# Performance work log

Measured on AMD Instinct MI355X. Metric: run time of the kernel, lower is better.

Reference implementation:

```python
import jax, jax.numpy as jnp
import numpy as np

N, D, Q, C_IN, C = 8192, 32, 4096, 128, 256
EPS = 1e-5

def _bn(h, g, b):
    # training-mode BatchNorm1d (biased variance, as torch uses for normalization)
    mu = h.mean(0)
    var = ((h - mu) ** 2).mean(0)
    return (h - mu) * jax.lax.rsqrt(var + EPS) * g + b

def setup_inputs():
    key = jax.random.key(0)
    cnt = iter(range(1000))
    def w(shape, s=0.05):
        return jax.random.normal(jax.random.fold_in(key, next(cnt)), shape, jnp.float32) * s
    ones = lambda n: jnp.ones((n,), jnp.float32)
    zeros = lambda n: jnp.zeros((n,), jnp.float32)
    rng = np.random.default_rng(0)
    block = N // D
    # padded neighbor table: rows sorted & duplicate-free (one neighbor per id-block)
    nbr_np = (np.arange(D)[None, :] * block + rng.integers(0, block, size=(N, D))).astype(np.int64)
    src = np.repeat(np.arange(N, dtype=np.int64), D)
    edge_index = jnp.asarray(np.stack([src, nbr_np.reshape(-1)]))
    E = edge_index.shape[1]
    C2 = 2 * C
    return {
        'x': w((N, C_IN), 1.0),
        'edge_index': edge_index,
        'edge_weight': jax.random.uniform(jax.random.fold_in(key, 999), (E,), jnp.float32, 0.5, 1.5),
        'edge_label_index': jnp.asarray(rng.integers(0, N, size=(2, Q)).astype(np.int64)),
        'nbr': jnp.asarray(nbr_np),
        'pe_gamma': ones(C_IN), 'pe_beta': zeros(C_IN),
        'W_pe': w((C_IN, C)), 'b_pe': zeros(C),
        'W_gcn': w((C, C)), 'b_gcn': zeros(C), 'bn1_g': ones(C), 'bn1_b': zeros(C),
        'Wq': w((C, C)), 'bq': zeros(C), 'Wk': w((C, C)), 'bk': zeros(C),
        'Wv': w((C, C)), 'bv': zeros(C), 'Wo': w((C, C)), 'bo': zeros(C),
        'bn2_g': ones(C), 'bn2_b': zeros(C),
        'W_m1': w((C, C2)), 'b_m1': zeros(C2), 'W_m2': w((C2, C)), 'b_m2': zeros(C),
        'bn3_g': ones(C), 'bn3_b': zeros(C),
        'W_cm': w((C, C)), 'b_cm': zeros(C), 'W_sm': w((C, C)), 'b_sm': zeros(C),
        'W_o1': w((C2, C)), 'b_o1': zeros(C), 'bno_g': ones(C), 'bno_b': zeros(C),
        'W_o2': w((C, 1)), 'b_o2': zeros(1),
        't': jnp.ones((), jnp.float32),
    }

def reference(x, edge_index, edge_weight, edge_label_index, nbr,
              pe_gamma, pe_beta, W_pe, b_pe,
              W_gcn, b_gcn, bn1_g, bn1_b,
              Wq, bq, Wk, bk, Wv, bv, Wo, bo, bn2_g, bn2_b,
              W_m1, b_m1, W_m2, b_m2, bn3_g, bn3_b,
              W_cm, b_cm, W_sm, b_sm,
              W_o1, b_o1, bno_g, bno_b, W_o2, b_o2, t):
    src, dst = edge_index[0], edge_index[1]
    h = _bn(x, pe_gamma, pe_beta) @ W_pe + b_pe                       # [N, C]
    # --- GPSConv layer: local GCN (self-loops) + global attention + MLP ---
    deg = jnp.zeros((N,), h.dtype).at[dst].add(edge_weight) + 1.0     # self-loop weight 1
    dinv = jax.lax.rsqrt(deg)
    hw = h @ W_gcn
    coef = dinv[src] * edge_weight * dinv[dst]
    agg = jnp.zeros_like(hw).at[dst].add(hw[src] * coef[:, None])
    local = agg + hw * (dinv * dinv)[:, None] + b_gcn
    h1 = _bn(local + h, bn1_g, bn1_b)
    q = h @ Wq + bq; k = h @ Wk + bk; v = h @ Wv + bv
    attn = jax.nn.softmax((q @ k.T) / jnp.sqrt(jnp.float32(C)), axis=-1)  # [N, N]
    h2 = _bn((attn @ v) @ Wo + bo + h, bn2_g, bn2_b)
    z = h1 + h2
    z = _bn(z + jax.nn.relu(z @ W_m1 + b_m1) @ W_m2 + b_m2, bn3_g, bn3_b)  # content features
    # --- structure: common-neighbor intersection + per-channel softmax aggregation ---
    s_nbr = nbr[edge_label_index[1]]        # [Q, D] sorted neighbors of source
    t_nbr = nbr[edge_label_index[0]]        # [Q, D] sorted neighbors of target
    pos = jnp.minimum(jax.vmap(jnp.searchsorted)(s_nbr, t_nbr), D - 1)
    mask = jnp.take_along_axis(s_nbr, pos, axis=1) == t_nbr           # common-neighbor mask
    zg = z[t_nbr]                           # [Q, D, C]
    m3 = mask[:, :, None]
    scores = jnp.where(m3, t * zg, -1e30)
    e = jnp.where(m3, jnp.exp(scores - jnp.max(scores, axis=1, keepdims=True)), 0.0)
    alpha = e / jnp.maximum(e.sum(axis=1, keepdims=True), 1e-12)
    structure = (alpha * zg).sum(axis=1)    # [Q, C]; zero rows when no common nbrs
    # --- predictor ---
    content = z[edge_label_index[0]] * z[edge_label_index[1]]
    hcat = jnp.concatenate([content @ W_cm + b_cm, structure @ W_sm + b_sm], axis=-1)
    hmid = jax.nn.relu(_bn(hcat @ W_o1 + b_o1, bno_g, bno_b))
    return hmid @ W_o2 + b_o2               # [Q, 1]
```

## Files before the change

### kernel.cpp

```cpp
#include <hip/hip_runtime.h>
#include <hip/hip_bf16.h>

using bf16 = __hip_bfloat16;
typedef __attribute__((ext_vector_type(8))) short short8;
typedef __attribute__((ext_vector_type(4))) float f32x4;
typedef __attribute__((ext_vector_type(4))) unsigned short us4;

#define NN 8192
#define DD 32
#define QQ 4096
#define CINN 128
#define CH 256
#define EE (NN*DD)
#define MBYTE ((size_t)1024*1024)
#define KB ((size_t)1024)

__device__ __forceinline__ short f2bf(float f){
  bf16 h = __float2bfloat16(f);
  return *reinterpret_cast<short*>(&h);
}
__device__ __forceinline__ float bf2f(unsigned short s){
  unsigned int u = ((unsigned int)s) << 16;
  return __uint_as_float(u);
}
__device__ __forceinline__ void gl_lds16(const void* g, void* l){
  __builtin_amdgcn_global_load_lds(
      (const __attribute__((address_space(1))) void*)g,
      (__attribute__((address_space(3))) void*)l, 16, 0, 0);
}

struct WPack {
  const float* src[11];
  bf16* dst[11];
  int K[11];
  int N[11];
  float sc[11];
  int cum[12];
};
__global__ void k_prepw(WPack p, float* stats, int nstats, int* cnt,
                        const float* __restrict__ bq, const float* __restrict__ bk,
                        const float* __restrict__ bv, float* __restrict__ bcat){
  int i = blockIdx.x*256 + threadIdx.x;
  if (i < 1024){
    float v = 0.f;
    if (i >= 768)      v = bv[i-768];
    else if (i >= 512) v = bk[i-512];
    else if (i >= 256) v = bq[i-256]*0.0625f;
    bcat[i] = v;
    return;
  }
  int j = i - 1024;
  if (j < nstats){ stats[j] = 0.f; return; }
  int k2 = j - nstats;
  if (k2 < NN){ cnt[k2] = 0; return; }
  int idx = k2 - NN;
  if (idx >= p.cum[11]) return;
  int w = 0;
#pragma unroll
  for (int t = 1; t < 11; t++) w += (idx >= p.cum[t]) ? 1 : 0;
  int loc = idx - p.cum[w];
  int K = p.K[w], N = p.N[w];
  int n = loc / K, k = loc - n*K;
  p.dst[w][loc] = __float2bfloat16(p.src[w][(size_t)k*N + n] * p.sc[w]);
}

__global__ void k_bnstats(const float* __restrict__ X, float* __restrict__ sums, int M, int C){
  int c = threadIdx.x;
  float s = 0.f, s2 = 0.f;
  for (int r = blockIdx.x; r < M; r += gridDim.x){
    float v = X[(size_t)r*C + c];
    s += v; s2 += v*v;
  }
  atomicAdd(&sums[c], s);
  atomicAdd(&sums[C+c], s2);
}

__global__ void k_bnstats_b(const bf16* __restrict__ X, float* __restrict__ sums, int M, int C){
  int c = threadIdx.x;
  float s = 0.f, s2 = 0.f;
  for (int r = blockIdx.x; r < M; r += gridDim.x){
    float v = __bfloat162float(X[(size_t)r*C + c]);
    s += v; s2 += v*v;
  }
  atomicAdd(&sums[c], s);
  atomicAdd(&sums[C+c], s2);
}

__global__ void k_bnapply(const float* __restrict__ X, const float* __restrict__ sums,
                          const float* __restrict__ g, const float* __restrict__ b,
                          bf16* __restrict__ outb, int M, int Cm1){
  int idx = blockIdx.x*256 + threadIdx.x;
  int c = idx & Cm1;
  int C = Cm1 + 1;
  float mu = sums[c] / (float)M;
  float var = sums[C+c] / (float)M - mu*mu;
  float rs = rsqrtf(var + 1e-5f);
  float v = (X[idx] - mu)*rs*g[c] + b[c];
  outb[idx] = __float2bfloat16(v);
}

__global__ void k_bnz(const float* __restrict__ y2, const float* __restrict__ stat2,
                      const float* __restrict__ g2, const float* __restrict__ b2,
                      const bf16* __restrict__ y1b, const float* __restrict__ stat1,
                      const float* __restrict__ g1, const float* __restrict__ b1,
                      bf16* __restrict__ zb){
  int idx = blockIdx.x*256 + threadIdx.x;
  int c = idx & 255;
  float mu2 = stat2[c] / (float)NN;
  float var2 = stat2[CH+c] / (float)NN - mu2*mu2;
  float rs2 = rsqrtf(var2 + 1e-5f);
  float v2 = (y2[idx] - mu2)*rs2*g2[c] + b2[c];
  float mu1 = stat1[c] / (float)NN;
  float var1 = stat1[CH+c] / (float)NN - mu1*mu1;
  float rs1 = rsqrtf(var1 + 1e-5f);
  float v1 = (__bfloat162float(y1b[idx]) - mu1)*rs1*g1[c] + b1[c];
  zb[idx] = __float2bfloat16(v1 + v2);
}

template<int KCH>
__global__ __launch_bounds__(256)
void k_gemm(const bf16* __restrict__ A, const bf16* __restrict__ BT,
            const float* __restrict__ bias,
            bf16* __restrict__ Cb, int ldc,
            const bf16* __restrict__ A2, const bf16* __restrict__ BT2,
            const float* __restrict__ bias2, int half, int colbase2)
{
  constexpr int K = KCH*32;
  int bid = blockIdx.x;
  const bf16* Ause = A;
  const bf16* BTu = BT;
  const float* bi = bias;
  int colbase = 0;
  if (A2 && bid >= half){ Ause = A2; BTu = BT2; bi = bias2; bid -= half; colbase = colbase2; }
  const int row0 = bid*16;
  const int wid = threadIdx.x >> 6;
  const int lane = threadIdx.x & 63;
  const int lr = lane & 15, lg = lane >> 4;
  short8 af[KCH];
  const short* Arow = (const short*)Ause + (size_t)(row0+lr)*K + lg*8;
#pragma unroll
  for (int c2 = 0; c2 < KCH; c2++) af[c2] = *(const short8*)(Arow + c2*32);
  const int ntiles = 256 >> 4;
  for (int ct = wid; ct < ntiles; ct += 4){
    f32x4 acc = {0.f,0.f,0.f,0.f};
    const short* Brow = (const short*)BTu + (size_t)(ct*16+lr)*K + lg*8;
#pragma unroll
    for (int c2 = 0; c2 < KCH; c2++){
      short8 bfr = *(const short8*)(Brow + c2*32);
      acc = __builtin_amdgcn_mfma_f32_16x16x32_bf16(af[c2], bfr, acc, 0, 0, 0);
    }
    int col = colbase + ct*16 + lr;
    float bvv = bi ? bi[ct*16+lr] : 0.f;
#pragma unroll
    for (int r = 0; r < 4; r++){
      int row = row0 + lg*4 + r;
      size_t o = (size_t)row*ldc + col;
      float v = acc[r] + bvv;
      Cb[o] = __float2bfloat16(v);
    }
  }
}

template<int KCH>
__global__ __launch_bounds__(256)
void k_gemm2(const bf16* __restrict__ A, const bf16* __restrict__ BT,
             const float* __restrict__ bias,
             const float* __restrict__ resid, const bf16* __restrict__ residb,
             float* __restrict__ Cf, bf16* __restrict__ Cb,
             int ncolsh, int ldc, int relu,
             int halfblocks, int colshift,
             float* __restrict__ stats)
{
  constexpr int K = KCH*32;
  int bid = blockIdx.x;
  int colbase = 0;
  if (bid >= halfblocks){ bid -= halfblocks; colbase = colshift; }
  const int row0 = bid*32;
  const int wid = threadIdx.x >> 6;
  const int lane = threadIdx.x & 63;
  const int lr = lane & 15, lg = lane >> 4;
  short8 af0[KCH], af1[KCH];
  const short* Arow0 = (const short*)A + (size_t)(row0+lr)*K + lg*8;
  const short* Arow1 = Arow0 + 16*K;
#pragma unroll
  for (int c2 = 0; c2 < KCH; c2++){
    af0[c2] = *(const short8*)(Arow0 + c2*32);
    af1[c2] = *(const short8*)(Arow1 + c2*32);
  }
  const int ntiles = ncolsh >> 4;
  for (int ct = wid; ct < ntiles; ct += 4){
    f32x4 a0 = {0.f,0.f,0.f,0.f}, a1 = {0.f,0.f,0.f,0.f};
    const short* Brow = (const short*)BT + (size_t)(colbase + ct*16 + lr)*K + lg*8;
#pragma unroll
    for (int c2 = 0; c2 < KCH; c2++){
      short8 bfr = *(const short8*)(Brow + c2*32);
      a0 = __builtin_amdgcn_mfma_f32_16x16x32_bf16(af0[c2], bfr, a0, 0, 0, 0);
      a1 = __builtin_amdgcn_mfma_f32_16x16x32_bf16(af1[c2], bfr, a1, 0, 0, 0);
    }
    int col = colbase + ct*16 + lr;
    float bvv = bias ? bias[col] : 0.f;
    float vv0[4], vv1[4];
#pragma unroll
    for (int r = 0; r < 4; r++){
      int row = row0 + lg*4 + r;
      size_t o0 = (size_t)row*ldc + col;
      size_t o1 = (size_t)(row+16)*ldc + col;
      float v0 = a0[r] + bvv;
      float v1 = a1[r] + bvv;
      if (resid){ v0 += resid[o0]; v1 += resid[o1]; }
      if (residb){ v0 += __bfloat162float(residb[o0]); v1 += __bfloat162float(residb[o1]); }
      if (relu){ v0 = fmaxf(v0, 0.f); v1 = fmaxf(v1, 0.f); }
      if (Cf){ Cf[o0] = v0; Cf[o1] = v1; }
      if (Cb){ Cb[o0] = __float2bfloat16(v0); Cb[o1] = __float2bfloat16(v1); }
      vv0[r] = v0; vv1[r] = v1;
    }
    if (stats){
      float s  = vv0[0]+vv0[1]+vv0[2]+vv0[3] + vv1[0]+vv1[1]+vv1[2]+vv1[3];
      float s2 = vv0[0]*vv0[0]+vv0[1]*vv0[1]+vv0[2]*vv0[2]+vv0[3]*vv0[3]
               + vv1[0]*vv1[0]+vv1[1]*vv1[1]+vv1[2]*vv1[2]+vv1[3]*vv1[3];
      s  += __shfl_xor(s, 16, 64);  s  += __shfl_xor(s, 32, 64);
      s2 += __shfl_xor(s2, 16, 64); s2 += __shfl_xor(s2, 32, 64);
      if (lg == 0){
        atomicAdd(&stats[col], s);
        atomicAdd(&stats[CH + col], s2);
      }
    }
  }
}

__global__ void k_hist(const int* __restrict__ dst, int* __restrict__ cnt){
  int e = blockIdx.x*256 + threadIdx.x;
  if (e < EE) atomicAdd(&cnt[dst[e]], 1);
}

__global__ void k_scan(const int* __restrict__ cnt, int* __restrict__ off, int* __restrict__ woff){
  __shared__ int s[256];
  int t = threadIdx.x;
  int base = t*32;
  int local[32];
  int sum = 0;
#pragma unroll
  for (int i = 0; i < 32; i++){ local[i] = sum; sum += cnt[base+i]; }
  s[t] = sum;
  __syncthreads();
  if (t == 0){
    int run = 0;
    for (int i = 0; i < 256; i++){ int v = s[i]; s[i] = run; run += v; }
  }
  __syncthreads();
  int b = s[t];
#pragma unroll
  for (int i = 0; i < 32; i++){ off[base+i] = b + local[i]; woff[base+i] = b + local[i]; }
  if (t == 255) off[8192] = EE;
}

__global__ void k_fill(const int* __restrict__ dst, int* __restrict__ woff, int* __restrict__ elist){
  int e = blockIdx.x*256 + threadIdx.x;
  if (e < EE){
    int p = atomicAdd(&woff[dst[e]], 1);
    elist[p] = e;
  }
}

__global__ __launch_bounds__(256)
void k_degcsr(const int* __restrict__ off, const int* __restrict__ elist,
              const float* __restrict__ ew, float* __restrict__ dinv){
  int n = blockIdx.x*4 + (threadIdx.x >> 6);
  int lane = threadIdx.x & 63;
  int o0 = off[n], o1 = off[n+1];
  float s = 0.f;
  for (int j = o0 + lane; j < o1; j += 64) s += ew[elist[j]];
#pragma unroll
  for (int o = 32; o; o >>= 1) s += __shfl_xor(s, o, 64);
  if (lane == 0) dinv[n] = rsqrtf(s + 1.0f);
}

__global__ __launch_bounds__(256)
void k_gather(const int* __restrict__ off, const int* __restrict__ elist,
              const float* __restrict__ ew, const float* __restrict__ dinv,
              const unsigned short* __restrict__ hwq, const unsigned short* __restrict__ hb16,
              const float* __restrict__ bgcn, bf16* __restrict__ y1b){
  int n = blockIdx.x*4 + (threadIdx.x >> 6);
  int lane = threadIdx.x & 63;
  int o0 = off[n], o1 = off[n+1];
  float dn = dinv[n];
  f32x4 acc = {0.f,0.f,0.f,0.f};
  for (int j = o0; j < o1; j++){
    int e = elist[j];
    int s = e >> 5;
    float coef = dinv[s]*ew[e]*dn;
    us4 v = *(const us4*)(hwq + (size_t)s*1024 + lane*4);
    acc[0] += bf2f(v[0])*coef; acc[1] += bf2f(v[1])*coef;
    acc[2] += bf2f(v[2])*coef; acc[3] += bf2f(v[3])*coef;
  }
  us4 hv = *(const us4*)(hwq + (size_t)n*1024 + lane*4);
  us4 hn = *(const us4*)(hb16 + (size_t)n*CH + lane*4);
  f32x4 bg  = ((const f32x4*)bgcn)[lane];
  float dd = dn*dn;
  us4 o;
  o[0] = (unsigned short)f2bf(acc[0] + bf2f(hv[0])*dd + bg[0] + bf2f(hn[0]));
  o[1] = (unsigned short)f2bf(acc[1] + bf2f(hv[1])*dd + bg[1] + bf2f(hn[1]));
  o[2] = (unsigned short)f2bf(acc[2] + bf2f(hv[2])*dd + bg[2] + bf2f(hn[2]));
  o[3] = (unsigned short)f2bf(acc[3] + bf2f(hv[3])*dd + bg[3] + bf2f(hn[3]));
  *(us4*)((unsigned short*)y1b + (size_t)n*CH + lane*4) = o;
}

__global__ __launch_bounds__(256)
void k_transpose(const bf16* __restrict__ in, bf16* __restrict__ out, int istride){
  __shared__ short tile[32][33];
  int bx = blockIdx.x & 7;
  int by = blockIdx.x >> 3;
  int tx = threadIdx.x & 31, ty = threadIdx.x >> 5;
  const short* inp = (const short*)in;
  short* outp = (short*)out;
#pragma unroll
  for (int i = 0; i < 4; i++)
    tile[ty + i*8][tx] = inp[(size_t)(by*32 + ty + i*8)*istride + bx*32 + tx];
  __syncthreads();
#pragma unroll
  for (int i = 0; i < 4; i++)
    outp[(size_t)(bx*32 + ty + i*8)*8192 + by*32 + tx] = tile[tx][ty + i*8];
}

__global__ __launch_bounds__(256, 2)
void k_attn9(const bf16* __restrict__ QKV, const bf16* __restrict__ VT,
             bf16* __restrict__ Opart, float* __restrict__ Lpart)
{
  __shared__ char lds[75776];
  const int wid = threadIdx.x >> 6, lane = threadIdx.x & 63;
  const int lr = lane & 15, lg = lane >> 4;
  const int qt = blockIdx.x >> 3, sp = blockIdx.x & 7;
  const int q0 = qt*128 + wid*32;
  const int kbase = sp*1024;
  const float M0 = 8.f;

  short8 qf[2][8];
#pragma unroll
  for (int qs = 0; qs < 2; qs++){
    const short* Qrow = (const short*)QKV + 256 + (size_t)(q0 + qs*16 + lr)*1024 + lg*8;
#pragma unroll
    for (int c = 0; c < 8; c++) qf[qs][c] = *(const short8*)(Qrow + c*32);
  }

  const char* kS[4];
  const char* vS[4];
  int ldst[4];
#pragma unroll
  for (int i = 0; i < 4; i++){
    int L = wid*1024 + i*4096 + lane*16;
    int r = L >> 9, b = L & 511;
    kS[i] = (const char*)QKV + (size_t)(kbase + r)*2048 + 1024 + (b ^ ((r&7)<<4));
    int j = L >> 7, b2 = L & 127;
    int bp2 = b2 ^ ((j&7)<<4);
    int dim = 2*j + (bp2 >= 64 ? 1 : 0);
    vS[i] = (const char*)VT + ((size_t)dim*8192 + kbase)*2 + (bp2 & 63);
    ldst[i] = wid*1024 + i*4096;
  }

  f32x4 acc[2][16];
#pragma unroll
  for (int qs = 0; qs < 2; qs++)
#pragma unroll
    for (int dt = 0; dt < 16; dt++) acc[qs][dt] = {0.f,0.f,0.f,0.f};
  float ls[2][4];
#pragma unroll
  for (int qs = 0; qs < 2; qs++)
#pragma unroll
    for (int r = 0; r < 4; r++) ls[qs][r] = 0.f;

  char* sPw = lds + 65536 + wid*2560;

#pragma unroll
  for (int i = 0; i < 4; i++){
    gl_lds16(kS[i], lds + ldst[i]);           kS[i] += 65536;
    gl_lds16(vS[i], lds + 16384 + ldst[i]);   vS[i] += 64;
  }
  __syncthreads();

  for (int t = 0; t < 32; t++){
    const int buf = t & 1;
    if (t < 31){
      char* nb = lds + (buf^1)*32768;
#pragma unroll
      for (int i = 0; i < 4; i++){
        gl_lds16(kS[i], nb + ldst[i]);           kS[i] += 65536;
        gl_lds16(vS[i], nb + 16384 + ldst[i]);   vS[i] += 64;
      }
    }
    const char* bK = lds + buf*32768;
    const char* bV = bK + 16384;

    {
      f32x4 s0 = {0.f,0.f,0.f,0.f}, s1 = {0.f,0.f,0.f,0.f};
      __builtin_amdgcn_s_setprio(1);
#pragma unroll
      for (int c = 0; c < 8; c++){
        int g = c*64 + lg*16;
        short8 kf0 = *(const short8*)(bK + lr*512 + (g ^ ((lr&7)<<4)));
        s0 = __builtin_amdgcn_mfma_f32_16x16x32_bf16(qf[0][c], kf0, s0, 0, 0, 0);
        short8 kf1 = *(const short8*)(bK + (16+lr)*512 + (g ^ ((lr&7)<<4)));
        s1 = __builtin_amdgcn_mfma_f32_16x16x32_bf16(qf[0][c], kf1, s1, 0, 0, 0);
      }
      __builtin_amdgcn_s_setprio(0);
#pragma unroll
      for (int r = 0; r < 4; r++){
        float p0 = __expf(s0[r] - M0);
        float p1 = __expf(s1[r] - M0);
        ls[0][r] += p0 + p1;
        int prow = lg*4 + r;
        *(short*)(sPw + prow*80 + lr*2)      = f2bf(p0);
        *(short*)(sPw + prow*80 + 32 + lr*2) = f2bf(p1);
      }
    }
    {
      f32x4 s0 = {0.f,0.f,0.f,0.f}, s1 = {0.f,0.f,0.f,0.f};
      __builtin_amdgcn_s_setprio(1);
#pragma unroll
      for (int c = 0; c < 8; c++){
        int g = c*64 + lg*16;
        short8 kf0 = *(const short8*)(bK + lr*512 + (g ^ ((lr&7)<<4)));
        s0 = __builtin_amdgcn_mfma_f32_16x16x32_bf16(qf[1][c], kf0, s0, 0, 0, 0);
        short8 kf1 = *(const short8*)(bK + (16+lr)*512 + (g ^ ((lr&7)<<4)));
        s1 = __builtin_amdgcn_mfma_f32_16x16x32_bf16(qf[1][c], kf1, s1, 0, 0, 0);
      }
      __builtin_amdgcn_s_setprio(0);
#pragma unroll
      for (int r = 0; r < 4; r++){
        float p0 = __expf(s0[r] - M0);
        float p1 = __expf(s1[r] - M0);
        ls[1][r] += p0 + p1;
        int prow = lg*4 + r;
        *(short*)(sPw + 1280 + prow*80 + lr*2)      = f2bf(p0);
        *(short*)(sPw + 1280 + prow*80 + 32 + lr*2) = f2bf(p1);
      }
    }
    __builtin_amdgcn_sched_barrier(0);
    short8 pf0 = *(const short8*)(sPw + lr*80 + lg*16);
    short8 pf1 = *(const short8*)(sPw + 1280 + lr*80 + lg*16);
    __builtin_amdgcn_s_setprio(1);
#pragma unroll
    for (int dt = 0; dt < 16; dt++){
      int d = dt*16 + lr;
      int j = d >> 1;
      int gp = (d&1)*64 + lg*16;
      short8 vf = *(const short8*)(bV + j*128 + (gp ^ ((j&7)<<4)));
      acc[0][dt] = __builtin_amdgcn_mfma_f32_16x16x32_bf16(pf0, vf, acc[0][dt], 0, 0, 0);
      acc[1][dt] = __builtin_amdgcn_mfma_f32_16x16x32_bf16(pf1, vf, acc[1][dt], 0, 0, 0);
    }
    __builtin_amdgcn_s_setprio(0);
    __syncthreads();
  }

#pragma unroll
  for (int qs = 0; qs < 2; qs++){
#pragma unroll
    for (int r = 0; r < 4; r++){
#pragma unroll
      for (int off = 1; off < 16; off <<= 1) ls[qs][r] += __shfl_xor(ls[qs][r], off, 64);
    }
  }
  if (lr == 0){
#pragma unroll
    for (int qs = 0; qs < 2; qs++){
#pragma unroll
      for (int r = 0; r < 4; r++){
        int row = q0 + qs*16 + lg*4 + r;
        Lpart[sp*NN + row] = ls[qs][r];
      }
    }
  }
  char* reg = lds + wid*8192;
  size_t ob = (size_t)sp*NN*CH;
#pragma unroll
  for (int qs = 0; qs < 2; qs++){
#pragma unroll
    for (int dt = 0; dt < 16; dt++){
#pragma unroll
      for (int r = 0; r < 4; r++){
        int qr = lg*4 + r;
        *(short*)(reg + qr*512 + ((dt*32 + lr*2) ^ ((qr&7)<<4))) = f2bf(acc[qs][dt][r]);
      }
    }
    __syncthreads();
#pragma unroll
    for (int rnd = 0; rnd < 8; rnd++){
      int qr = rnd*2 + (lane >> 5);
      int colb = (lane & 31)*16;
      short8 v = *(const short8*)(reg + qr*512 + (colb ^ ((qr&7)<<4)));
      *(short8*)((short*)Opart + ob + (size_t)(q0 + qs*16 + qr)*CH + colb/2) = v;
    }
    __syncthreads();
  }
}

__global__ __launch_bounds__(256)
void k_merge8(const bf16* __restrict__ Opart, const float* __restrict__ Lp,
              bf16* __restrict__ out){
  int tid = blockIdx.x*256 + threadIdx.x;
  int q = tid >> 5;
  int cb = (tid & 31) * 8;
  float den = 0.f;
#pragma unroll
  for (int s = 0; s < 8; s++) den += Lp[s*NN + q];
  float inv = 1.f / den;
  float o[8];
#pragma unroll
  for (int j = 0; j < 8; j++) o[j] = 0.f;
#pragma unroll
  for (int s = 0; s < 8; s++){
    short8 v = *(const short8*)((const short*)Opart + (size_t)s*NN*CH + (size_t)q*CH + cb);
#pragma unroll
    for (int j = 0; j < 8; j++) o[j] += bf2f((unsigned short)v[j]);
  }
  short8 res;
#pragma unroll
  for (int j = 0; j < 8; j++) res[j] = f2bf(o[j]*inv);
  *(short8*)((short*)out + (size_t)q*CH + cb) = res;
}

__global__ __launch_bounds__(256)
void k_head(const int* __restrict__ eli, const int* __restrict__ nbr,
            const float* __restrict__ y3, const float* __restrict__ stat3,
            const float* __restrict__ g3, const float* __restrict__ b3,
            const float* __restrict__ tptr,
            bf16* __restrict__ outc, bf16* __restrict__ outs){
  __shared__ int tn[32];
  __shared__ int msk[32];
  int q = blockIdx.x;
  int a0 = eli[q], b0 = eli[QQ + q];
  if (threadIdx.x < 32){
    int d = threadIdx.x;
    int a = nbr[(size_t)a0*DD + d];
    int s = nbr[(size_t)b0*DD + d];
    tn[d] = a;
    msk[d] = (a == s);
  }
  __syncthreads();
  int c = threadIdx.x;
  float mu = stat3[c] / (float)NN;
  float var = stat3[CH + c] / (float)NN - mu*mu;
  float rs = rsqrtf(var + 1e-5f);
  float sc = rs*g3[c];
  float sh = b3[c] - mu*sc;
  float za = y3[(size_t)a0*CH + c]*sc + sh;
  float zb = y3[(size_t)b0*CH + c]*sc + sh;
  outc[(size_t)q*CH + c] = __float2bfloat16(za*zb);
  float tval = tptr[0];
  float vmax = -1e30f;
  float zg[32];
#pragma unroll
  for (int d = 0; d < 32; d++){
    float v = msk[d] ? (y3[(size_t)tn[d]*CH + c]*sc + sh) : 0.f;
    zg[d] = v;
    float scv = msk[d] ? tval*v : -1e30f;
    vmax = fmaxf(vmax, scv);
  }
  float esum = 0.f, wsum = 0.f;
#pragma unroll
  for (int d = 0; d < 32; d++){
    float e = msk[d] ? __expf(tval*zg[d] - vmax) : 0.f;
    esum += e;
    wsum += e*zg[d];
  }
  outs[(size_t)q*CH + c] = __float2bfloat16(wsum / fmaxf(esum, 1e-12f));
}

__global__ __launch_bounds__(256)
void k_final(const float* __restrict__ y4, const float* __restrict__ stato,
             const float* __restrict__ g, const float* __restrict__ b,
             const float* __restrict__ w, const float* __restrict__ bo2,
             float* __restrict__ out){
  int r = blockIdx.x*4 + (threadIdx.x >> 6);
  int lane = threadIdx.x & 63;
  float s = 0.f;
#pragma unroll
  for (int i = 0; i < 4; i++){
    int c = lane + 64*i;
    float mu = stato[c] / (float)QQ;
    float var = stato[CH+c] / (float)QQ - mu*mu;
    float rs = rsqrtf(var + 1e-5f);
    float v = (y4[(size_t)r*CH + c] - mu)*rs*g[c] + b[c];
    v = fmaxf(v, 0.f);
    s += v * w[c];
  }
#pragma unroll
  for (int off = 32; off; off >>= 1) s += __shfl_xor(s, off, 64);
  if (lane == 0) out[r] = s + bo2[0];
}

extern "C" void kernel_launch(void* const* d_in, const int* in_sizes, int n_in,
                              void* d_out, int out_size, void* d_ws, size_t ws_size,
                              hipStream_t stream)
{
  const float* x      = (const float*)d_in[0];
  const int*   eidx   = (const int*)d_in[1];
  const float* ew     = (const float*)d_in[2];
  const int*   eli    = (const int*)d_in[3];
  const int*   nbr    = (const int*)d_in[4];
  const float* pe_g   = (const float*)d_in[5];
  const float* pe_b   = (const float*)d_in[6];
  const float* W_pe   = (const float*)d_in[7];
  const float* b_pe   = (const float*)d_in[8];
  const float* W_gcn  = (const float*)d_in[9];
  const float* b_gcn  = (const float*)d_in[10];
  const float* bn1_g  = (const float*)d_in[11];
  const float* bn1_b  = (const float*)d_in[12];
  const float* Wq     = (const float*)d_in[13];
  const float* bq     = (const float*)d_in[14];
  const float* Wk     = (const float*)d_in[15];
  const float* bk     = (const float*)d_in[16];
  const float* Wv     = (const float*)d_in[17];
  const float* bvv    = (const float*)d_in[18];
  const float* Wo     = (const float*)d_in[19];
  const float* bo     = (const float*)d_in[20];
  const float* bn2_g  = (const float*)d_in[21];
  const float* bn2_b  = (const float*)d_in[22];
  const float* W_m1   = (const float*)d_in[23];
  const float* b_m1   = (const float*)d_in[24];
  const float* W_m2   = (const float*)d_in[25];
  const float* b_m2   = (const float*)d_in[26];
  const float* bn3_g  = (const float*)d_in[27];
  const float* bn3_b  = (const float*)d_in[28];
  const float* W_cm   = (const float*)d_in[29];
  const float* b_cm   = (const float*)d_in[30];
  const float* W_sm   = (const float*)d_in[31];
  const float* b_sm   = (const float*)d_in[32];
  const float* W_o1   = (const float*)d_in[33];
  const float* b_o1   = (const float*)d_in[34];
  const float* bno_g  = (const float*)d_in[35];
  const float* bno_b  = (const float*)d_in[36];
  const float* W_o2   = (const float*)d_in[37];
  const float* b_o2   = (const float*)d_in[38];
  const float* tptr   = (const float*)d_in[39];

  if (ws_size < 64*MBYTE) return;
  char* ws = (char*)d_ws;

  bf16* WgcnT = (bf16*)(ws + 0);
  bf16* WqT   = (bf16*)(ws + 128*KB);
  bf16* WkT   = (bf16*)(ws + 256*KB);
  bf16* WvT   = (bf16*)(ws + 384*KB);
  bf16* WpeT  = (bf16*)(ws + 512*KB);
  bf16* Wm1T  = (bf16*)(ws + 576*KB);
  bf16* Wm2T  = (bf16*)(ws + 832*KB);
  bf16* WcmT  = (bf16*)(ws + 1088*KB);
  bf16* WsmT  = (bf16*)(ws + 1216*KB);
  bf16* Wo1T  = (bf16*)(ws + 1344*KB);
  bf16* WoT   = (bf16*)(ws + 1600*KB);

  float* stat_x = (float*)(ws + 2*MBYTE);
  float* stat1  = (float*)(ws + 2*MBYTE + 1*KB);
  float* stat2  = (float*)(ws + 2*MBYTE + 3*KB);
  float* stat3  = (float*)(ws + 2*MBYTE + 5*KB);
  float* stato  = (float*)(ws + 2*MBYTE + 7*KB);
  float* deg    = (float*)(ws + 2*MBYTE + 16*KB);
  float* bcat   = (float*)(ws + 2*MBYTE + 64*KB);
  int*   cnt    = (int*)(ws + 2*MBYTE + 128*KB);
  int*   off    = (int*)(ws + 2*MBYTE + 160*KB);
  int*   woff   = (int*)(ws + 2*MBYTE + 224*KB);
  int*   elist  = (int*)(ws + 2*MBYTE + 288*KB);
  float* Lpart  = (float*)(ws + 2*MBYTE + 1664*KB);

  bf16*  hb    = (bf16*)(ws + 4*MBYTE);
  bf16*  xn    = (bf16*)(ws + 8*MBYTE);
  bf16*  OpartB= (bf16*)(ws + 8*MBYTE);
  bf16*  vT    = (bf16*)(ws + 40*MBYTE);
  bf16*  qkvg  = (bf16*)(ws + 44*MBYTE);
  bf16*  y1b   = (bf16*)(ws + 60*MBYTE);
  bf16*  attnb = (bf16*)(ws + 40*MBYTE);
  float* y2    = (float*)(ws + 8*MBYTE);
  bf16*  zb    = (bf16*)(ws + 24*MBYTE);
  bf16*  midb  = (bf16*)(ws + 28*MBYTE);
  float* y3    = (float*)(ws + 44*MBYTE);
  bf16*  contb = (bf16*)(ws + 8*MBYTE);
  bf16*  strub = (bf16*)(ws + 10*MBYTE);
  bf16*  hcat  = (bf16*)(ws + 12*MBYTE);
  float* y4    = (float*)(ws + 16*MBYTE);

  const int* dstp = eidx + EE;

  {
    WPack p;
    const float* s[11] = {W_gcn, Wq, Wk, Wv, W_pe, W_m1, W_m2, W_cm, W_sm, W_o1, Wo};
    bf16* dsts[11] = {WgcnT, WqT, WkT, WvT, WpeT, Wm1T, Wm2T, WcmT, WsmT, Wo1T, WoT};
    int Ks[11] = {256,256,256,256,128,256,512,256,256,512,256};
    int Ns[11] = {256,256,256,256,256,512,256,256,256,256,256};
    float scs[11] = {1.f,0.0625f,1.f,1.f,1.f,1.f,1.f,1.f,1.f,1.f,1.f};
    int c = 0;
    for (int i = 0; i < 11; i++){
      p.src[i]=s[i]; p.dst[i]=dsts[i]; p.K[i]=Ks[i]; p.N[i]=Ns[i]; p.sc[i]=scs[i];
      p.cum[i]=c; c += Ks[i]*Ns[i];
    }
    p.cum[11]=c;
    int total = 1024 + 12288 + NN + c;
    k_prepw<<<(total+255)/256, 256, 0, stream>>>(p, (float*)(ws + 2*MBYTE), 12288, cnt, bq, bk, bvv, bcat);
  }

  k_hist<<<EE/256, 256, 0, stream>>>(dstp, cnt);
  k_scan<<<1, 256, 0, stream>>>(cnt, off, woff);
  k_fill<<<EE/256, 256, 0, stream>>>(dstp, woff, elist);
  k_degcsr<<<NN/4, 256, 0, stream>>>(off, elist, ew, deg);

  k_bnstats<<<256, 128, 0, stream>>>(x, stat_x, NN, CINN);
  k_bnapply<<<NN*CINN/256, 256, 0, stream>>>(x, stat_x, pe_g, pe_b, xn, NN, CINN-1);

  k_gemm2<4><<<512, 256, 0, stream>>>(xn, WpeT, b_pe, nullptr, nullptr, nullptr, hb, 128, 256, 0,
                                       256, 128, nullptr);

  k_gemm2<8><<<512, 256, 0, stream>>>(hb, WgcnT, bcat, nullptr, nullptr, nullptr, qkvg, 512, 1024, 0,
                                       256, 512, nullptr);

  k_gather<<<NN/4, 256, 0, stream>>>(off, elist, ew, deg,
                                      (const unsigned short*)qkvg, (const unsigned short*)hb, b_gcn, y1b);

  k_bnstats_b<<<256, 256, 0, stream>>>(y1b, stat1, NN, CH);

  k_transpose<<<2048, 256, 0, stream>>>(qkvg + 768, vT, 1024);

  k_attn9<<<512, 256, 0, stream>>>(qkvg, vT, OpartB, Lpart);
  k_merge8<<<NN*32/256, 256, 0, stream>>>(OpartB, Lpart, attnb);

  k_gemm2<8><<<512, 256, 0, stream>>>(attnb, WoT, bo, nullptr, hb, y2, nullptr, 128, 256, 0,
                                       256, 128, stat2);

  k_bnz<<<NN*CH/256, 256, 0, stream>>>(y2, stat2, bn2_g, bn2_b, y1b, stat1, bn1_g, bn1_b, zb);

  k_gemm2<8><<<512, 256, 0, stream>>>(zb, Wm1T, b_m1, nullptr, nullptr, nullptr, midb, 256, 512, 1,
                                       256, 256, nullptr);
  k_gemm2<16><<<512, 256, 0, stream>>>(midb, Wm2T, b_m2, nullptr, zb, y3, nullptr, 128, 256, 0,
                                        256, 128, stat3);

  k_head<<<QQ, 256, 0, stream>>>(eli, nbr, y3, stat3, bn3_g, bn3_b, tptr, contb, strub);

  k_gemm<8><<<2*(QQ/16), 256, 0, stream>>>(contb, WcmT, b_cm, hcat, 512,
                                            strub, WsmT, b_sm, QQ/16, 256);

  k_gemm2<16><<<256, 256, 0, stream>>>(hcat, Wo1T, b_o1, nullptr, nullptr, y4, nullptr, 128, 256, 0,
                                        128, 128, stato);

  k_final<<<QQ/4, 256, 0, stream>>>(y4, stato, bno_g, bno_b, W_o2, b_o2, (float*)d_out);
}
```

Measured before the change: 360.1 us.

## Fuse attention split merge into output projection GEMM and store y3 as bf16

Removes the separate merge kernel. A new GEMM kernel now reduces the eight attention partial outputs, normalizes them by the summed softmax denominators in registers, and feeds the result straight into MFMA for the Wo projection with residual, bias and BN stats. This saves one kernel launch and the write and read of the merged attention tensor. Separately, y3 is now stored as bf16 instead of fp32, which halves the bytes the head kernel gathers. The cost is that each column-half block redoes the partial merge (the Opart reads are doubled), and y3 loses precision before the BN3 normalization.

```diff
diff --git a/kernel.cpp b/kernel.cpp
--- a/kernel.cpp
+++ b/kernel.cpp
@@ -228,6 +228,82 @@
   }
 }
 
+__global__ __launch_bounds__(256)
+void k_gemmW(const bf16* __restrict__ Opart, const float* __restrict__ Lp,
+             const bf16* __restrict__ BT, const float* __restrict__ bias,
+             const bf16* __restrict__ residb, float* __restrict__ Cf,
+             float* __restrict__ stats)
+{
+  constexpr int K = 256;
+  int bid = blockIdx.x;
+  int colbase = 0;
+  if (bid >= 256){ bid -= 256; colbase = 128; }
+  const int row0 = bid*32;
+  const int wid = threadIdx.x >> 6;
+  const int lane = threadIdx.x & 63;
+  const int lr = lane & 15, lg = lane >> 4;
+  const int ra = row0 + lr, rb = row0 + 16 + lr;
+  float dena = 0.f, denb = 0.f;
+#pragma unroll
+  for (int s = 0; s < 8; s++){ dena += Lp[s*NN + ra]; denb += Lp[s*NN + rb]; }
+  float inva = 1.f/dena, invb = 1.f/denb;
+  short8 af0[8], af1[8];
+#pragma unroll
+  for (int c2 = 0; c2 < 8; c2++){
+    float aa[8] = {0.f,0.f,0.f,0.f,0.f,0.f,0.f,0.f};
+    float ab[8] = {0.f,0.f,0.f,0.f,0.f,0.f,0.f,0.f};
+#pragma unroll
+    for (int s = 0; s < 8; s++){
+      short8 va = *(const short8*)((const short*)Opart + (size_t)s*NN*CH + (size_t)ra*CH + lg*8 + c2*32);
+      short8 vb = *(const short8*)((const short*)Opart + (size_t)s*NN*CH + (size_t)rb*CH + lg*8 + c2*32);
+#pragma unroll
+      for (int j = 0; j < 8; j++){
+        aa[j] += bf2f((unsigned short)va[j]);
+        ab[j] += bf2f((unsigned short)vb[j]);
+      }
+    }
+#pragma unroll
+    for (int j = 0; j < 8; j++){
+      af0[c2][j] = f2bf(aa[j]*inva);
+      af1[c2][j] = f2bf(ab[j]*invb);
+    }
+  }
+  const int ntiles = 8;
+  for (int ct = wid; ct < ntiles; ct += 4){
+    f32x4 a0 = {0.f,0.f,0.f,0.f}, a1 = {0.f,0.f,0.f,0.f};
+    const short* Brow = (const short*)BT + (size_t)(colbase + ct*16 + lr)*K + lg*8;
+#pragma unroll
+    for (int c2 = 0; c2 < 8; c2++){
+      short8 bfr = *(const short8*)(Brow + c2*32);
+      a0 = __builtin_amdgcn_mfma_f32_16x16x32_bf16(af0[c2], bfr, a0, 0, 0, 0);
+      a1 = __builtin_amdgcn_mfma_f32_16x16x32_bf16(af1[c2], bfr, a1, 0, 0, 0);
+    }
+    int col = colbase + ct*16 + lr;
+    float bvv = bias[col];
+    float vv0[4], vv1[4];
+#pragma unroll
+    for (int r = 0; r < 4; r++){
+      int row = row0 + lg*4 + r;
+      size_t o0 = (size_t)row*CH + col;
+      size_t o1 = (size_t)(row+16)*CH + col;
+      float v0 = a0[r] + bvv + __bfloat162float(residb[o0]);
+      float v1 = a1[r] + bvv + __bfloat162float(residb[o1]);
+      Cf[o0] = v0;
+      Cf[o1] = v1;
+      vv0[r] = v0; vv1[r] = v1;
+    }
+    float s  = vv0[0]+vv0[1]+vv0[2]+vv0[3] + vv1[0]+vv1[1]+vv1[2]+vv1[3];
+    float s2 = vv0[0]*vv0[0]+vv0[1]*vv0[1]+vv0[2]*vv0[2]+vv0[3]*vv0[3]
+             + vv1[0]*vv1[0]+vv1[1]*vv1[1]+vv1[2]*vv1[2]+vv1[3]*vv1[3];
+    s  += __shfl_xor(s, 16, 64);  s  += __shfl_xor(s, 32, 64);
+    s2 += __shfl_xor(s2, 16, 64); s2 += __shfl_xor(s2, 32, 64);
+    if (lg == 0){
+      atomicAdd(&stats[col], s);
+      atomicAdd(&stats[CH + col], s2);
+    }
+  }
+}
+
 __global__ void k_hist(const int* __restrict__ dst, int* __restrict__ cnt){
   int e = blockIdx.x*256 + threadIdx.x;
   if (e < EE) atomicAdd(&cnt[dst[e]], 1);
@@ -494,33 +570,8 @@
 }
 
 __global__ __launch_bounds__(256)
-void k_merge8(const bf16* __restrict__ Opart, const float* __restrict__ Lp,
-              bf16* __restrict__ out){
-  int tid = blockIdx.x*256 + threadIdx.x;
-  int q = tid >> 5;
-  int cb = (tid & 31) * 8;
-  float den = 0.f;
-#pragma unroll
-  for (int s = 0; s < 8; s++) den += Lp[s*NN + q];
-  float inv = 1.f / den;
-  float o[8];
-#pragma unroll
-  for (int j = 0; j < 8; j++) o[j] = 0.f;
-#pragma unroll
-  for (int s = 0; s < 8; s++){
-    short8 v = *(const short8*)((const short*)Opart + (size_t)s*NN*CH + (size_t)q*CH + cb);
-#pragma unroll
-    for (int j = 0; j < 8; j++) o[j] += bf2f((unsigned short)v[j]);
-  }
-  short8 res;
-#pragma unroll
-  for (int j = 0; j < 8; j++) res[j] = f2bf(o[j]*inv);
-  *(short8*)((short*)out + (size_t)q*CH + cb) = res;
-}
-
-__global__ __launch_bounds__(256)
 void k_head(const int* __restrict__ eli, const int* __restrict__ nbr,
-            const float* __restrict__ y3, const float* __restrict__ stat3,
+            const bf16* __restrict__ y3b, const float* __restrict__ stat3,
             const float* __restrict__ g3, const float* __restrict__ b3,
             const float* __restrict__ tptr,
             bf16* __restrict__ outc, bf16* __restrict__ outs){
@@ -542,15 +593,15 @@
   float rs = rsqrtf(var + 1e-5f);
   float sc = rs*g3[c];
   float sh = b3[c] - mu*sc;
-  float za = y3[(size_t)a0*CH + c]*sc + sh;
-  float zb = y3[(size_t)b0*CH + c]*sc + sh;
+  float za = __bfloat162float(y3b[(size_t)a0*CH + c])*sc + sh;
+  float zb = __bfloat162float(y3b[(size_t)b0*CH + c])*sc + sh;
   outc[(size_t)q*CH + c] = __float2bfloat16(za*zb);
   float tval = tptr[0];
   float vmax = -1e30f;
   float zg[32];
 #pragma unroll
   for (int d = 0; d < 32; d++){
-    float v = msk[d] ? (y3[(size_t)tn[d]*CH + c]*sc + sh) : 0.f;
+    float v = msk[d] ? (__bfloat162float(y3b[(size_t)tn[d]*CH + c])*sc + sh) : 0.f;
     zg[d] = v;
     float scv = msk[d] ? tval*v : -1e30f;
     vmax = fmaxf(vmax, scv);
@@ -667,11 +718,10 @@
   bf16*  vT    = (bf16*)(ws + 40*MBYTE);
   bf16*  qkvg  = (bf16*)(ws + 44*MBYTE);
   bf16*  y1b   = (bf16*)(ws + 60*MBYTE);
-  bf16*  attnb = (bf16*)(ws + 40*MBYTE);
-  float* y2    = (float*)(ws + 8*MBYTE);
+  float* y2    = (float*)(ws + 44*MBYTE);
   bf16*  zb    = (bf16*)(ws + 24*MBYTE);
   bf16*  midb  = (bf16*)(ws + 28*MBYTE);
-  float* y3    = (float*)(ws + 44*MBYTE);
+  bf16*  y3b   = (bf16*)(ws + 52*MBYTE);
   bf16*  contb = (bf16*)(ws + 8*MBYTE);
   bf16*  strub = (bf16*)(ws + 10*MBYTE);
   bf16*  hcat  = (bf16*)(ws + 12*MBYTE);
@@ -718,19 +768,17 @@
   k_transpose<<<2048, 256, 0, stream>>>(qkvg + 768, vT, 1024);
 
   k_attn9<<<512, 256, 0, stream>>>(qkvg, vT, OpartB, Lpart);
-  k_merge8<<<NN*32/256, 256, 0, stream>>>(OpartB, Lpart, attnb);
-
-  k_gemm2<8><<<512, 256, 0, stream>>>(attnb, WoT, bo, nullptr, hb, y2, nullptr, 128, 256, 0,
-                                       256, 128, stat2);
+
+  k_gemmW<<<512, 256, 0, stream>>>(OpartB, Lpart, WoT, bo, hb, y2, stat2);
 
   k_bnz<<<NN*CH/256, 256, 0, stream>>>(y2, stat2, bn2_g, bn2_b, y1b, stat1, bn1_g, bn1_b, zb);
 
   k_gemm2<8><<<512, 256, 0, stream>>>(zb, Wm1T, b_m1, nullptr, nullptr, nullptr, midb, 256, 512, 1,
                                        256, 256, nullptr);
-  k_gemm2<16><<<512, 256, 0, stream>>>(midb, Wm2T, b_m2, nullptr, zb, y3, nullptr, 128, 256, 0,
+  k_gemm2<16><<<512, 256, 0, stream>>>(midb, Wm2T, b_m2, nullptr, zb, nullptr, y3b, 128, 256, 0,
                                         256, 128, stat3);
 
-  k_head<<<QQ, 256, 0, stream>>>(eli, nbr, y3, stat3, bn3_g, bn3_b, tptr, contb, strub);
+  k_head<<<QQ, 256, 0, stream>>>(eli, nbr, y3b, stat3, bn3_g, bn3_b, tptr, contb, strub);
 
   k_gemm<8><<<2*(QQ/16), 256, 0, stream>>>(contb, WcmT, b_cm, hcat, 512,
                                             strub, WsmT, b_sm, QQ/16, 256);
```

Result: slower. 372.6 us (+3.5%).
